# Optimization experiments

Measured on AMD Instinct MI355X. Metric: run time of the kernel, lower is better.

Reference implementation:

```python
import jax, jax.numpy as jnp
import numpy as np

NUM_HEADS = 12

def setup_inputs() -> dict:
    key = jax.random.key(0)
    k1, k2, k3, k4 = jax.random.split(key, 4)
    B, T, N, C = 8, 16, 196, 768
    x = jax.random.normal(k1, (B, T, N, C), dtype=jnp.float32)
    # qkv Linear (no bias): stored as [C, 3C] so y = x @ W_qkv
    W_qkv = jax.random.normal(k2, (C, 3 * C), dtype=jnp.float32) * (C ** -0.5)
    W_proj = jax.random.normal(k3, (C, C), dtype=jnp.float32) * (C ** -0.5)
    b_proj = jax.random.normal(k4, (C,), dtype=jnp.float32) * 0.02
    return {"x": x, "W_qkv": W_qkv, "W_proj": W_proj, "b_proj": b_proj}

def reference(x, W_qkv, W_proj, b_proj):
    B, T, N, C = x.shape
    H = NUM_HEADS
    hd = C // H
    scale = hd ** -0.5
    # shared QKV projection -> [3, B, T, H, N, hd]
    qkv = (x @ W_qkv).reshape(B, T, N, 3, H, hd).transpose(3, 0, 1, 4, 2, 5)
    q, k, v = qkv[0], qkv[1], qkv[2]
    # spatial attention over N (per frame)
    attn = jax.nn.softmax(jnp.einsum('bthnd,bthmd->bthnm', q, k) * scale, axis=-1)
    x1 = jnp.einsum('bthnm,bthmd->bthnd', attn, v)
    x1 = x1.transpose(0, 1, 3, 2, 4).reshape(B, T, N, C)  # [B,T,N,H,hd]->[B,T,N,C]
    # temporal attention over T (per spatial token): permute to [B,H,N,T,hd]
    q2 = q.transpose(0, 2, 3, 1, 4)
    k2 = k.transpose(0, 2, 3, 1, 4)
    v2 = v.transpose(0, 2, 3, 1, 4)
    attn2 = jax.nn.softmax(jnp.einsum('bhntd,bhnsd->bhnts', q2, k2) * scale, axis=-1)
    x2 = jnp.einsum('bhnts,bhnsd->bhntd', attn2, v2)
    x2 = x2.transpose(0, 3, 2, 1, 4).reshape(B, T, N, C)  # [B,T,N,H,hd]->[B,T,N,C]
    # average the two branches, then output projection
    return ((x1 + x2) * 0.5) @ W_proj + b_proj
```

## Files before the change

kernel.cpp:

```cpp
#include <hip/hip_runtime.h>
#include <cstdint>
#include <cstddef>

typedef unsigned short ushort_t;
typedef unsigned int   uint_t;

#define B_   8
#define T_   16
#define N_   196
#define C_   768
#define H_   12
#define C3_  2304
#define M_   25088

#define NP_  208
#define KS_  72
#define VS_  232
#define PS_  232

#define TS_  40

typedef __attribute__((ext_vector_type(8))) short short8;
typedef __attribute__((ext_vector_type(4))) float floatx4;

__device__ __forceinline__ float bf2f(ushort_t u) {
  return __uint_as_float(((uint_t)u) << 16);
}
__device__ __forceinline__ ushort_t f2bf(float f) {
  uint_t u = __float_as_uint(f);
  u += 0x7FFFu + ((u >> 16) & 1u);
  return (ushort_t)(u >> 16);
}
__device__ __forceinline__ uint_t pack2(float a, float b) {
  return (uint_t)f2bf(a) | ((uint_t)f2bf(b) << 16);
}

__device__ __forceinline__ void gload_lds16(const ushort_t* g, ushort_t* l) {
  __builtin_amdgcn_global_load_lds(
      (const __attribute__((address_space(1))) uint_t*)g,
      (__attribute__((address_space(3))) uint_t*)l, 16, 0, 0);
}

__device__ __forceinline__ void bar() {
  asm volatile("" ::: "memory");
  __builtin_amdgcn_s_barrier();
  __builtin_amdgcn_sched_barrier(0);
}

__global__ void fsta_prep(const float* __restrict__ x,
                          ushort_t* __restrict__ xbf,
                          const float* __restrict__ Wqkv,
                          ushort_t* __restrict__ WtQkv,
                          const float* __restrict__ Wproj,
                          ushort_t* __restrict__ WtProj)
{
  __shared__ float tile[32][33];
  const int bid = blockIdx.x;
  const int tid = threadIdx.x;
  if (bid < 9408) {
    int i = (bid * 256 + tid) * 8;
    const float* f = x + i;
    uint4 u;
    u.x = pack2(f[0], f[1]); u.y = pack2(f[2], f[3]);
    u.z = pack2(f[4], f[5]); u.w = pack2(f[6], f[7]);
    *(uint4*)(xbf + i) = u;
    return;
  }
  const float* src; ushort_t* dst; int Cc, rt, ct;
  if (bid < 11136) {
    int b2 = bid - 9408;
    src = Wqkv; dst = WtQkv; Cc = 2304; ct = b2 % 72; rt = b2 / 72;
  } else {
    int b2 = bid - 11136;
    src = Wproj; dst = WtProj; Cc = 768; ct = b2 % 24; rt = b2 / 24;
  }
  const int tx = tid & 31, ty = tid >> 5;
#pragma unroll
  for (int i = 0; i < 4; ++i)
    tile[ty + i * 8][tx] =
        src[(size_t)(rt * 32 + ty + i * 8) * Cc + ct * 32 + tx];
  __syncthreads();
#pragma unroll
  for (int i = 0; i < 4; ++i)
    dst[(size_t)(ct * 32 + ty + i * 8) * 768 + rt * 32 + tx] =
        f2bf(tile[tx][ty + i * 8]);
}

#define STG(X, rb, bu, xo, kss, t)                                            \
  { _Pragma("unroll") for (int c_ = 0; c_ < 2; ++c_) {                        \
      const ushort_t* g_ = (X) +                                              \
          (size_t)((rb) + c_ * 128 + wv * 16 + srow) * K +                    \
          (t) * 64 + (kss) * 32 + chnk * 8;                                   \
      gload_lds16(g_, &lds[(bu) * 32768 + (xo) + (kss) * 8192 +               \
                           c_ * 4096 + wv * 512]); } }

#define PH(bu, mh, kss, DOB, GUARD, ...)                                      \
  { short8 af[4];                                                             \
    _Pragma("unroll") for (int m2 = 0; m2 < 4; ++m2) {                        \
      int rr = wm * 128 + ((mh) * 4 + m2) * 16 + lrow;                        \
      af[m2] = *(const short8*)&lds[(bu) * 32768 + (kss) * 8192 +             \
                                    rr * 32 + rch8]; }                        \
    if (DOB) {                                                                \
      _Pragma("unroll") for (int n2 = 0; n2 < 4; ++n2) {                      \
        int rr = wn * 64 + n2 * 16 + lrow;                                    \
        bf[n2] = *(const short8*)&lds[(bu) * 32768 + 16384 + (kss) * 8192 +   \
                                      rr * 32 + rch8]; } }                    \
    __VA_ARGS__                                                               \
    GUARD                                                                     \
    bar();                                                                    \
    __builtin_amdgcn_s_setprio(1);                                            \
    _Pragma("unroll") for (int m2 = 0; m2 < 4; ++m2)                          \
      _Pragma("unroll") for (int n2 = 0; n2 < 4; ++n2)                        \
        acc[(mh) * 4 + m2][n2] = __builtin_amdgcn_mfma_f32_16x16x32_bf16(     \
            af[m2], bf[n2], acc[(mh) * 4 + m2][n2], 0, 0, 0);                 \
    __builtin_amdgcn_s_setprio(0);                                            \
    bar(); }

#define GUARD_NONE
#define GUARD4 asm volatile("s_waitcnt vmcnt(4)" ::: "memory");
#define GUARD0 asm volatile("s_waitcnt vmcnt(0)" ::: "memory");

template <typename OutT>
__global__ __launch_bounds__(512) void fsta_gemm256(
    const ushort_t* __restrict__ A1,
    const ushort_t* __restrict__ Bt,
    const float* __restrict__ bias,
    OutT* __restrict__ Cout,
    int Ncols, int K)
{
  __shared__ ushort_t lds[65536];
  const int tid  = threadIdx.x;
  const int lane = tid & 63;
  const int wv   = tid >> 6;
  const int wm   = wv >> 2;
  const int wn   = wv & 3;
  const int lrow = lane & 15;
  const int quad = lane >> 4;
  const int rch8 = (quad ^ ((lrow >> 1) & 3)) * 8;
  const int srow = lane >> 2;
  const int chnk = (lane & 3) ^ ((srow >> 1) & 3);

  const int ntx = gridDim.x;
  const int gdy = gridDim.y;
  const int nwg = ntx * gdy;
  int lin = blockIdx.y * ntx + blockIdx.x;
  {
    int q = nwg >> 3, r = nwg & 7;
    int xcd = lin & 7, off = lin >> 3;
    lin = (xcd < r ? xcd * (q + 1) : r * (q + 1) + (xcd - r) * q) + off;
  }
  const int m0 = (lin / gdy) * 256;
  const int n0 = (lin % gdy) * 256;

  const int NT = K >> 6;
  const int NI = NT >> 1;

  floatx4 acc[8][4];
#pragma unroll
  for (int i = 0; i < 8; ++i)
#pragma unroll
    for (int j = 0; j < 4; ++j)
      acc[i][j] = (floatx4){0.f, 0.f, 0.f, 0.f};

  STG(A1, m0, 0, 0,     0, 0)
  STG(Bt, n0, 0, 16384, 0, 0)
  STG(A1, m0, 0, 0,     1, 0)
  STG(Bt, n0, 0, 16384, 1, 0)
  STG(A1, m0, 1, 0,     0, 1)
  STG(Bt, n0, 1, 16384, 0, 1)
  GUARD4
  bar();

  short8 bf[4];
  for (int i = 0; i < NI; ++i) {
    const int t0 = 2 * i;
    const bool lastI = (i == NI - 1);
    PH(0, 0, 0, 1, GUARD_NONE,
       { STG(A1, m0, 1, 0, 1, t0 + 1) STG(Bt, n0, 1, 16384, 1, t0 + 1) })
    PH(0, 1, 0, 0, GUARD_NONE, )
    PH(0, 0, 1, 1, GUARD_NONE,
       { if (!lastI) { STG(A1, m0, 0, 0, 0, t0 + 2) } })
    PH(0, 1, 1, 0, if (lastI) { GUARD0 } else { GUARD4 },
       { if (!lastI) { STG(Bt, n0, 0, 16384, 0, t0 + 2) } })
    PH(1, 0, 0, 1, GUARD_NONE,
       { if (!lastI) { STG(A1, m0, 0, 0, 1, t0 + 2)
                       STG(Bt, n0, 0, 16384, 1, t0 + 2) } })
    PH(1, 1, 0, 0, GUARD_NONE, )
    PH(1, 0, 1, 1, GUARD_NONE,
       { if (!lastI) { STG(A1, m0, 1, 0, 0, t0 + 3) } })
    PH(1, 1, 1, 0, if (!lastI) { GUARD4 },
       { if (!lastI) { STG(Bt, n0, 1, 16384, 0, t0 + 3) } })
  }

#pragma unroll
  for (int m2 = 0; m2 < 8; ++m2) {
    int row = m0 + wm * 128 + m2 * 16 + quad * 4;
#pragma unroll
    for (int n2 = 0; n2 < 4; ++n2) {
      int col = n0 + wn * 64 + n2 * 16 + lrow;
      float badd = bias ? bias[col] : 0.f;
#pragma unroll
      for (int rr = 0; rr < 4; ++rr) {
        float v = acc[m2][n2][rr] + badd;
        if constexpr (sizeof(OutT) == 4)
          Cout[(size_t)(row + rr) * Ncols + col] = v;
        else
          Cout[(size_t)(row + rr) * Ncols + col] = (OutT)f2bf(v);
      }
    }
  }
}

__global__ __launch_bounds__(832) void fsta_spatial(
    const ushort_t* __restrict__ qkv, ushort_t* __restrict__ x1)
{
  __shared__ ushort_t Ks[NP_ * KS_];
  __shared__ ushort_t Vt[64 * VS_];
  __shared__ ushort_t Ps[13][16 * PS_];
  const int tid = threadIdx.x;
  const int bid = blockIdx.x;
  const int h   = bid % H_;
  const int bt  = bid / H_;
  const size_t rowbase = (size_t)bt * N_ * C3_;
  const int hofs = h * 64;

  for (int idx = tid; idx < N_ * 8; idx += 832) {
    int n = idx >> 3, c = (idx & 7) * 8;
    size_t so = rowbase + (size_t)n * C3_ + hofs + c;
    *(uint4*)&Ks[n * KS_ + c] = *(const uint4*)(qkv + so + 768);
    uint4 v = *(const uint4*)(qkv + so + 1536);
    ushort_t tmp[8];
    *(uint4*)tmp = v;
#pragma unroll
    for (int i = 0; i < 8; ++i) Vt[(c + i) * VS_ + n] = tmp[i];
  }
  for (int idx = tid; idx < 64 * (VS_ - N_); idx += 832) {
    int d = idx / (VS_ - N_), k = N_ + idx % (VS_ - N_);
    Vt[d * VS_ + k] = 0;
  }
  __syncthreads();

  const int lane = tid & 63;
  const int qt   = tid >> 6;
  const int lrow = lane & 15;
  const int quad = lane >> 4;
  const int k8   = quad * 8;

  {
    int qrow = qt * 16 + lrow; if (qrow > N_ - 1) qrow = N_ - 1;
    const ushort_t* qp = qkv + rowbase + (size_t)qrow * C3_ + hofs;
    short8 qf0 = *(const short8*)(qp + k8);
    short8 qf1 = *(const short8*)(qp + 32 + k8);

    floatx4 s[13];
#pragma unroll
    for (int kt = 0; kt < 13; ++kt) {
      const ushort_t* kp = &Ks[(kt * 16 + lrow) * KS_];
      short8 kf0 = *(const short8*)(kp + k8);
      short8 kf1 = *(const short8*)(kp + 32 + k8);
      floatx4 a = (floatx4){0.f, 0.f, 0.f, 0.f};
      a = __builtin_amdgcn_mfma_f32_16x16x32_bf16(qf0, kf0, a, 0, 0, 0);
      a = __builtin_amdgcn_mfma_f32_16x16x32_bf16(qf1, kf1, a, 0, 0, 0);
      s[kt] = a;
    }

    if (lrow >= 4)
      s[12] = (floatx4){-INFINITY, -INFINITY, -INFINITY, -INFINITY};

    float mx[4], sum[4];
#pragma unroll
    for (int r = 0; r < 4; ++r) {
      float m2 = s[0][r];
#pragma unroll
      for (int kt = 1; kt < 13; ++kt) m2 = fmaxf(m2, s[kt][r]);
#pragma unroll
      for (int xm = 1; xm < 16; xm <<= 1) m2 = fmaxf(m2, __shfl_xor(m2, xm, 64));
      mx[r] = m2;
    }
#pragma unroll
    for (int r = 0; r < 4; ++r) {
      float sm = 0.f;
#pragma unroll
      for (int kt = 0; kt < 13; ++kt) {
        float p = __expf((s[kt][r] - mx[r]) * 0.125f);
        s[kt][r] = p;
        sm += p;
      }
#pragma unroll
      for (int xm = 1; xm < 16; xm <<= 1) sm += __shfl_xor(sm, xm, 64);
      sum[r] = sm;
    }

    ushort_t* pw = Ps[qt];
#pragma unroll
    for (int kt = 0; kt < 13; ++kt)
#pragma unroll
      for (int r = 0; r < 4; ++r)
        pw[(quad * 4 + r) * PS_ + kt * 16 + lrow] = f2bf(s[kt][r]);
#pragma unroll
    for (int r = 0; r < 4; ++r)
      pw[(quad * 4 + r) * PS_ + 208 + lrow] = 0;

    floatx4 o[4];
#pragma unroll
    for (int nt = 0; nt < 4; ++nt) o[nt] = (floatx4){0.f, 0.f, 0.f, 0.f};
#pragma unroll
    for (int kt = 0; kt < 7; ++kt) {
      short8 pf = *(const short8*)&pw[lrow * PS_ + kt * 32 + k8];
#pragma unroll
      for (int nt = 0; nt < 4; ++nt) {
        short8 vf = *(const short8*)&Vt[(nt * 16 + lrow) * VS_ + kt * 32 + k8];
        o[nt] = __builtin_amdgcn_mfma_f32_16x16x32_bf16(pf, vf, o[nt], 0, 0, 0);
      }
    }

    float inv[4];
#pragma unroll
    for (int r = 0; r < 4; ++r) inv[r] = 1.f / sum[r];
#pragma unroll
    for (int nt = 0; nt < 4; ++nt)
#pragma unroll
      for (int r = 0; r < 4; ++r)
        pw[(quad * 4 + r) * 64 + nt * 16 + lrow] = f2bf(o[nt][r] * inv[r]);
#pragma unroll
    for (int tr = 0; tr < 16; ++tr) {
      int qr = qt * 16 + tr;
      if (qr < N_)
        x1[(size_t)(bt * N_ + qr) * C_ + hofs + lane] = pw[tr * 64 + lane];
    }
  }
}

__global__ __launch_bounds__(256) void fsta_temporal(
    const ushort_t* __restrict__ qkv, ushort_t* __restrict__ xavg)
{
  __shared__ ushort_t Pt[4][16 * TS_];
  __shared__ ushort_t Vw[4][64 * TS_];
  __shared__ ushort_t Ot[4][16 * 64];
  const int tid  = threadIdx.x;
  const int lane = tid & 63;
  const int wv   = tid >> 6;
  const int gw   = blockIdx.x * 4 + wv;
  const int n    = gw % N_;
  const int bh   = gw / N_;
  const int h    = bh % H_;
  const int b    = bh / H_;
  const int hofs = h * 64;
  const int lrow = lane & 15;
  const int quad = lane >> 4;
  const int k8   = quad * 8;

  ushort_t* pw = Pt[wv];
  ushort_t* vw = Vw[wv];

  for (int i = lane; i < 16 * 16; i += 64)
    pw[(i >> 4) * TS_ + 16 + (i & 15)] = 0;
  for (int i = lane; i < 64 * 16; i += 64)
    vw[(i >> 4) * TS_ + 16 + (i & 15)] = 0;

  for (int i = lane; i < 128; i += 64) {
    int s = i >> 3, c8 = (i & 7) * 8;
    size_t vo = ((size_t)((b * T_ + s) * N_ + n)) * C3_ + hofs + 1536 + c8;
    ushort_t tmp[8];
    *(uint4*)tmp = *(const uint4*)(qkv + vo);
#pragma unroll
    for (int j = 0; j < 8; ++j) vw[(c8 + j) * TS_ + s] = tmp[j];
  }

  const size_t ro = ((size_t)((b * T_ + lrow) * N_ + n)) * C3_ + hofs;
  short8 qf0 = *(const short8*)(qkv + ro + k8);
  short8 qf1 = *(const short8*)(qkv + ro + 32 + k8);
  short8 kf0 = *(const short8*)(qkv + ro + 768 + k8);
  short8 kf1 = *(const short8*)(qkv + ro + 800 + k8);

  floatx4 s4 = (floatx4){0.f, 0.f, 0.f, 0.f};
  s4 = __builtin_amdgcn_mfma_f32_16x16x32_bf16(qf0, kf0, s4, 0, 0, 0);
  s4 = __builtin_amdgcn_mfma_f32_16x16x32_bf16(qf1, kf1, s4, 0, 0, 0);

  float inv[4];
#pragma unroll
  for (int r = 0; r < 4; ++r) {
    float m2 = s4[r];
#pragma unroll
    for (int xm = 1; xm < 16; xm <<= 1) m2 = fmaxf(m2, __shfl_xor(m2, xm, 64));
    float p = __expf((s4[r] - m2) * 0.125f);
    float sm = p;
#pragma unroll
    for (int xm = 1; xm < 16; xm <<= 1) sm += __shfl_xor(sm, xm, 64);
    pw[(quad * 4 + r) * TS_ + lrow] = f2bf(p);
    inv[r] = 1.f / sm;
  }

  short8 pf = *(const short8*)&pw[lrow * TS_ + k8];
  floatx4 o[4];
#pragma unroll
  for (int nt = 0; nt < 4; ++nt) {
    short8 vf = *(const short8*)&vw[(nt * 16 + lrow) * TS_ + k8];
    o[nt] = __builtin_amdgcn_mfma_f32_16x16x32_bf16(
        pf, vf, (floatx4){0.f, 0.f, 0.f, 0.f}, 0, 0, 0);
  }

  ushort_t* ow = Ot[wv];
#pragma unroll
  for (int nt = 0; nt < 4; ++nt)
#pragma unroll
    for (int r = 0; r < 4; ++r)
      ow[(quad * 4 + r) * 64 + nt * 16 + lrow] = f2bf(o[nt][r] * inv[r]);

  const size_t obase = ((size_t)(b * T_) * N_ + n) * C_ + hofs + lane;
#pragma unroll
  for (int t = 0; t < T_; ++t) {
    size_t xo = obase + (size_t)t * (N_ * C_);
    float prev = bf2f(xavg[xo]);
    xavg[xo] = f2bf(0.5f * (prev + bf2f(ow[t * 64 + lane])));
  }
}

extern "C" void kernel_launch(void* const* d_in, const int* in_sizes, int n_in,
                              void* d_out, int out_size, void* d_ws, size_t ws_size,
                              hipStream_t stream)
{
  (void)in_sizes; (void)n_in; (void)out_size; (void)ws_size;
  const float* x     = (const float*)d_in[0];
  const float* Wqkv  = (const float*)d_in[1];
  const float* Wproj = (const float*)d_in[2];
  const float* bproj = (const float*)d_in[3];
  float*    out = (float*)d_out;
  ushort_t* ws  = (ushort_t*)d_ws;

  ushort_t* WtQkv  = ws;
  ushort_t* WtProj = ws + 1769472;
  ushort_t* xbf    = ws + 2359296;
  ushort_t* xavg   = xbf;
  ushort_t* qkv    = ws + 21626880;

  fsta_prep<<<dim3(11712), dim3(256), 0, stream>>>(
      x, xbf, Wqkv, WtQkv, Wproj, WtProj);
  fsta_gemm256<ushort_t><<<dim3(98, 9), dim3(512), 0, stream>>>(
      xbf, WtQkv, (const float*)nullptr, qkv, 2304, 768);
  fsta_spatial<<<dim3(B_ * T_ * H_), dim3(832), 0, stream>>>(qkv, xavg);
  fsta_temporal<<<dim3((B_ * H_ * N_) / 4), dim3(256), 0, stream>>>(qkv, xavg);
  fsta_gemm256<float><<<dim3(98, 3), dim3(512), 0, stream>>>(
      xavg, WtProj, bproj, out, 768, 768);
}
```

Before: 394.8 us.

## Replace 256x256 GEMM with 128x128 tile, K=32 double-buffered kernel

Swaps the 512-thread 256x256-tile GEMM, which used an eight-phase interleaved pipeline, for a 256-thread 128x128-tile kernel. The new kernel uses a simple two-stage buffer with K steps of 32 and 32KB of LDS, and requests four blocks per CU through launch bounds. The goal is more workgroups and higher occupancy, which matters most for the small projection GEMM (294 tiles before). In exchange, operand reuse per tile drops, and a full vmcnt(0) wait every iteration can expose global load latency.

```diff
diff --git a/kernel.cpp b/kernel.cpp
--- a/kernel.cpp
+++ b/kernel.cpp
@@ -86,54 +86,30 @@
         f2bf(tile[tx][ty + i * 8]);
 }
 
-#define STG(X, rb, bu, xo, kss, t)                                            \
+#define STG1(X, rb, bu, xo, t)                                                \
   { _Pragma("unroll") for (int c_ = 0; c_ < 2; ++c_) {                        \
       const ushort_t* g_ = (X) +                                              \
-          (size_t)((rb) + c_ * 128 + wv * 16 + srow) * K +                    \
-          (t) * 64 + (kss) * 32 + chnk * 8;                                   \
-      gload_lds16(g_, &lds[(bu) * 32768 + (xo) + (kss) * 8192 +               \
-                           c_ * 4096 + wv * 512]); } }
-
-#define PH(bu, mh, kss, DOB, GUARD, ...)                                      \
-  { short8 af[4];                                                             \
-    _Pragma("unroll") for (int m2 = 0; m2 < 4; ++m2) {                        \
-      int rr = wm * 128 + ((mh) * 4 + m2) * 16 + lrow;                        \
-      af[m2] = *(const short8*)&lds[(bu) * 32768 + (kss) * 8192 +             \
-                                    rr * 32 + rch8]; }                        \
-    if (DOB) {                                                                \
-      _Pragma("unroll") for (int n2 = 0; n2 < 4; ++n2) {                      \
-        int rr = wn * 64 + n2 * 16 + lrow;                                    \
-        bf[n2] = *(const short8*)&lds[(bu) * 32768 + 16384 + (kss) * 8192 +   \
-                                      rr * 32 + rch8]; } }                    \
-    __VA_ARGS__                                                               \
-    GUARD                                                                     \
-    bar();                                                                    \
-    __builtin_amdgcn_s_setprio(1);                                            \
-    _Pragma("unroll") for (int m2 = 0; m2 < 4; ++m2)                          \
-      _Pragma("unroll") for (int n2 = 0; n2 < 4; ++n2)                        \
-        acc[(mh) * 4 + m2][n2] = __builtin_amdgcn_mfma_f32_16x16x32_bf16(     \
-            af[m2], bf[n2], acc[(mh) * 4 + m2][n2], 0, 0, 0);                 \
-    __builtin_amdgcn_s_setprio(0);                                            \
-    bar(); }
-
-#define GUARD_NONE
+          (size_t)((rb) + c_ * 64 + wv * 16 + srow) * K +                     \
+          (t) * 32 + chnk * 8;                                                \
+      gload_lds16(g_, &lds[(bu) * 8192 + (xo) + c_ * 2048 + wv * 512]); } }
+
 #define GUARD4 asm volatile("s_waitcnt vmcnt(4)" ::: "memory");
 #define GUARD0 asm volatile("s_waitcnt vmcnt(0)" ::: "memory");
 
 template <typename OutT>
-__global__ __launch_bounds__(512) void fsta_gemm256(
+__global__ __launch_bounds__(256, 4) void fsta_gemm128(
     const ushort_t* __restrict__ A1,
     const ushort_t* __restrict__ Bt,
     const float* __restrict__ bias,
     OutT* __restrict__ Cout,
     int Ncols, int K)
 {
-  __shared__ ushort_t lds[65536];
+  __shared__ ushort_t lds[16384];
   const int tid  = threadIdx.x;
   const int lane = tid & 63;
   const int wv   = tid >> 6;
-  const int wm   = wv >> 2;
-  const int wn   = wv & 3;
+  const int wm   = wv >> 1;
+  const int wn   = wv & 1;
   const int lrow = lane & 15;
   const int quad = lane >> 4;
   const int rch8 = (quad ^ ((lrow >> 1) & 3)) * 8;
@@ -149,52 +125,56 @@
     int xcd = lin & 7, off = lin >> 3;
     lin = (xcd < r ? xcd * (q + 1) : r * (q + 1) + (xcd - r) * q) + off;
   }
-  const int m0 = (lin / gdy) * 256;
-  const int n0 = (lin % gdy) * 256;
-
-  const int NT = K >> 6;
-  const int NI = NT >> 1;
-
-  floatx4 acc[8][4];
-#pragma unroll
-  for (int i = 0; i < 8; ++i)
+  const int m0 = (lin / gdy) * 128;
+  const int n0 = (lin % gdy) * 128;
+
+  const int NT = K >> 5;
+
+  floatx4 acc[4][4];
+#pragma unroll
+  for (int i = 0; i < 4; ++i)
 #pragma unroll
     for (int j = 0; j < 4; ++j)
       acc[i][j] = (floatx4){0.f, 0.f, 0.f, 0.f};
 
-  STG(A1, m0, 0, 0,     0, 0)
-  STG(Bt, n0, 0, 16384, 0, 0)
-  STG(A1, m0, 0, 0,     1, 0)
-  STG(Bt, n0, 0, 16384, 1, 0)
-  STG(A1, m0, 1, 0,     0, 1)
-  STG(Bt, n0, 1, 16384, 0, 1)
+  STG1(A1, m0, 0, 0,    0)
+  STG1(Bt, n0, 0, 4096, 0)
+  STG1(A1, m0, 1, 0,    1)
+  STG1(Bt, n0, 1, 4096, 1)
   GUARD4
   bar();
 
-  short8 bf[4];
-  for (int i = 0; i < NI; ++i) {
-    const int t0 = 2 * i;
-    const bool lastI = (i == NI - 1);
-    PH(0, 0, 0, 1, GUARD_NONE,
-       { STG(A1, m0, 1, 0, 1, t0 + 1) STG(Bt, n0, 1, 16384, 1, t0 + 1) })
-    PH(0, 1, 0, 0, GUARD_NONE, )
-    PH(0, 0, 1, 1, GUARD_NONE,
-       { if (!lastI) { STG(A1, m0, 0, 0, 0, t0 + 2) } })
-    PH(0, 1, 1, 0, if (lastI) { GUARD0 } else { GUARD4 },
-       { if (!lastI) { STG(Bt, n0, 0, 16384, 0, t0 + 2) } })
-    PH(1, 0, 0, 1, GUARD_NONE,
-       { if (!lastI) { STG(A1, m0, 0, 0, 1, t0 + 2)
-                       STG(Bt, n0, 0, 16384, 1, t0 + 2) } })
-    PH(1, 1, 0, 0, GUARD_NONE, )
-    PH(1, 0, 1, 1, GUARD_NONE,
-       { if (!lastI) { STG(A1, m0, 1, 0, 0, t0 + 3) } })
-    PH(1, 1, 1, 0, if (!lastI) { GUARD4 },
-       { if (!lastI) { STG(Bt, n0, 1, 16384, 0, t0 + 3) } })
-  }
-
-#pragma unroll
-  for (int m2 = 0; m2 < 8; ++m2) {
-    int row = m0 + wm * 128 + m2 * 16 + quad * 4;
+  for (int t = 0; t < NT; ++t) {
+    const int bu = t & 1;
+    short8 af[4], bfr[4];
+#pragma unroll
+    for (int m2 = 0; m2 < 4; ++m2)
+      af[m2] = *(const short8*)&lds[bu * 8192 +
+                                    (wm * 64 + m2 * 16 + lrow) * 32 + rch8];
+#pragma unroll
+    for (int n2 = 0; n2 < 4; ++n2)
+      bfr[n2] = *(const short8*)&lds[bu * 8192 + 4096 +
+                                     (wn * 64 + n2 * 16 + lrow) * 32 + rch8];
+    GUARD0
+    bar();
+    __builtin_amdgcn_s_setprio(1);
+#pragma unroll
+    for (int m2 = 0; m2 < 4; ++m2)
+#pragma unroll
+      for (int n2 = 0; n2 < 4; ++n2)
+        acc[m2][n2] = __builtin_amdgcn_mfma_f32_16x16x32_bf16(
+            af[m2], bfr[n2], acc[m2][n2], 0, 0, 0);
+    __builtin_amdgcn_s_setprio(0);
+    if (t + 2 < NT) {
+      STG1(A1, m0, bu, 0,    t + 2)
+      STG1(Bt, n0, bu, 4096, t + 2)
+    }
+    bar();
+  }
+
+#pragma unroll
+  for (int m2 = 0; m2 < 4; ++m2) {
+    int row = m0 + wm * 64 + m2 * 16 + quad * 4;
 #pragma unroll
     for (int n2 = 0; n2 < 4; ++n2) {
       int col = n0 + wn * 64 + n2 * 16 + lrow;
@@ -436,10 +416,10 @@
 
   fsta_prep<<<dim3(11712), dim3(256), 0, stream>>>(
       x, xbf, Wqkv, WtQkv, Wproj, WtProj);
-  fsta_gemm256<ushort_t><<<dim3(98, 9), dim3(512), 0, stream>>>(
+  fsta_gemm128<ushort_t><<<dim3(196, 18), dim3(256), 0, stream>>>(
       xbf, WtQkv, (const float*)nullptr, qkv, 2304, 768);
   fsta_spatial<<<dim3(B_ * T_ * H_), dim3(832), 0, stream>>>(qkv, xavg);
   fsta_temporal<<<dim3((B_ * H_ * N_) / 4), dim3(256), 0, stream>>>(qkv, xavg);
-  fsta_gemm256<float><<<dim3(98, 3), dim3(512), 0, stream>>>(
+  fsta_gemm128<float><<<dim3(196, 6), dim3(256), 0, stream>>>(
       xavg, WtProj, bproj, out, 768, 768);
 }
```

After: 389.1 us. About the same (-1.4%).
